# Performance work log

Hardware: AMD Instinct MI355X
Metric: run time of the kernel (lower is better)

The kernel has to match this reference:

```python
import jax, jax.numpy as jnp
import numpy as np

NEG_INF = -1e30  # stand-in for -inf that is safe under softmax
HEADS = 16


def slice_diag_idx(t):
    # result[i, j] = matrix[i, i + j] for matrix of shape (..., t, 2t-1)
    rows = jnp.arange(t)
    cols = rows[:, None] + rows[None, :]  # (t, t), values in [0, 2t-2]
    return rows, cols


def setup_inputs() -> dict:
    key = jax.random.key(0)
    ks = jax.random.split(key, 10)
    b, t, e, h = 4, 1024, 1024, HEADS
    s = e // h
    sc = 0.02
    return {
        "x": jax.random.normal(ks[0], (b, t, e), jnp.float32),
        "Wq": jax.random.normal(ks[1], (e, e), jnp.float32) * sc,
        "Wk": jax.random.normal(ks[2], (e, e), jnp.float32) * sc,
        "Wkp": jax.random.normal(ks[3], (e, e), jnp.float32) * sc,
        "Wv": jax.random.normal(ks[4], (e, e), jnp.float32) * sc,
        "Wu": jax.random.normal(ks[5], (e, e), jnp.float32) * sc,
        "bu": jax.random.normal(ks[6], (e,), jnp.float32) * sc,
        "parma": jax.random.normal(ks[7], (1, h, 1, s), jnp.float32),
        "parmb": jax.random.normal(ks[8], (1, h, 1, s), jnp.float32),
        "pos_emb": jax.random.normal(ks[9], (2 * t - 1, e), jnp.float32),
    }


def reference(x, Wq, Wk, Wkp, Wv, Wu, bu, parma, parmb, pos_emb):
    b, t, e = x.shape
    h = HEADS
    s = e // h

    q = (x @ Wq).reshape(b, t, h, s).transpose(0, 2, 1, 3)   # (b,h,t,s)
    k = (x @ Wk).reshape(b, t, h, s).transpose(0, 2, 1, 3)   # (b,h,t,s)
    v = (x @ Wv).reshape(b, t, h, s).transpose(0, 2, 1, 3)   # (b,h,t,s)
    # positions are identical across batch -> compute once, shape (2t-1,h,s)
    kp = (pos_emb @ Wkp).reshape(2 * t - 1, h, s)

    pa = parma[0, :, 0, :]  # (h,s), broadcast over query position i
    pb = parmb[0, :, 0, :]  # (h,s)

    rows, cols = slice_diag_idx(t)

    # content-content
    dot_tt = jnp.einsum('bhis,bhjs->bhij', q, k)                 # (b,h,t,t)
    # content-position, then slice_diag: [i,j] -> [i, i+j]
    dot_tp_full = jnp.einsum('bhis,jhs->bhij', q, kp)            # (b,h,t,2t-1)
    dot_tp = dot_tp_full[:, :, rows[:, None], cols]              # (b,h,t,t)
    # position-content: constant over query index i
    dot_pt = jnp.einsum('hs,bhjs->bhj', pa, k)[:, :, None, :]    # (b,h,1,t)
    # position-position: constant over i before slicing; slice gives c[i+j]
    c_pp = jnp.einsum('hs,jhs->hj', pb, kp)                      # (h,2t-1)
    dot_pp = c_pp[:, cols][None]                                 # (1,h,t,t)

    dot = dot_tt + dot_tp + dot_pt + dot_pp                      # (b,h,t,t)

    # causal mask: strict upper triangle (j > i) -> -inf
    causal = rows[:, None] >= rows[None, :]                      # (t,t)
    dot = jnp.where(causal[None, None], dot, NEG_INF)

    att = jax.nn.softmax(dot, axis=-1)
    out = jnp.einsum('bhij,bhjs->bhis', att, v)                  # (b,h,t,s)
    out = out.transpose(0, 2, 1, 3).reshape(b, t, e)
    return out @ Wu + bu
```

## Files before the change

kernel.cpp:

```cpp
#include <hip/hip_runtime.h>

typedef unsigned short u16;
typedef unsigned int   u32;
using bf16x8 = __attribute__((ext_vector_type(8))) __bf16;
using f32x4  = __attribute__((ext_vector_type(4))) float;
using u16x8  = __attribute__((ext_vector_type(8))) u16;

#define NEG_INF_F (-1e30f)

__device__ __forceinline__ u16 f2bf(float f) {
  u32 u = __float_as_uint(f);
  u32 r = (u + 0x7FFFu + ((u >> 16) & 1u)) >> 16;
  return (u16)r;
}

__device__ __forceinline__ void async_copy16(const void* g, void* lds) {
  __builtin_amdgcn_global_load_lds(
      (const __attribute__((address_space(1))) void*)g,
      (__attribute__((address_space(3))) void*)lds, 16, 0, 0);
}

__global__ __launch_bounds__(256) void cvt_bf16(const float* __restrict__ in,
                                                u16* __restrict__ out, int n4) {
  int i = blockIdx.x * 256 + threadIdx.x;
  if (i >= n4) return;
  float4 v = reinterpret_cast<const float4*>(in)[i];
  u16 o0 = f2bf(v.x), o1 = f2bf(v.y), o2 = f2bf(v.z), o3 = f2bf(v.w);
  ushort4 o = {o0, o1, o2, o3};
  reinterpret_cast<ushort4*>(out)[i] = o;
}

__global__ __launch_bounds__(256) void cvt_w_tr(
    const float* __restrict__ w0, const float* __restrict__ w1,
    const float* __restrict__ w2, const float* __restrict__ w3,
    const float* __restrict__ w4,
    u16* __restrict__ o0, u16* __restrict__ o1, u16* __restrict__ o2,
    u16* __restrict__ o3, u16* __restrict__ o4) {
  __shared__ float tile[64][65];
  const float* src; u16* dst;
  switch (blockIdx.z) {
    case 0: src = w0; dst = o0; break;
    case 1: src = w1; dst = o1; break;
    case 2: src = w2; dst = o2; break;
    case 3: src = w3; dst = o3; break;
    default: src = w4; dst = o4; break;
  }
  const int tid = threadIdx.x;
  const int r0 = blockIdx.y * 64;
  const int c0 = blockIdx.x * 64;
#pragma unroll
  for (int i = 0; i < 16; ++i) {
    int lin = tid + i * 256;
    int r = lin >> 6, c = lin & 63;
    tile[r][c] = src[(size_t)(r0 + r) * 1024 + c0 + c];
  }
  __syncthreads();
#pragma unroll
  for (int i = 0; i < 16; ++i) {
    int lin = tid + i * 256;
    int n = lin >> 6, k = lin & 63;
    dst[(size_t)(c0 + n) * 1024 + r0 + k] = f2bf(tile[k][n]);
  }
}

__global__ __launch_bounds__(512, 2) void gemm_qkvp(
    const u16* __restrict__ x_bf, const u16* __restrict__ pos_bf,
    const u16* __restrict__ BtQKV, const u16* __restrict__ BtKP,
    u16* __restrict__ qa, u16* __restrict__ qb, u16* __restrict__ kb,
    u16* __restrict__ vb, u16* __restrict__ kp,
    const float* __restrict__ parma, const float* __restrict__ parmb) {
  const int bx = blockIdx.x, by = blockIdx.y;
  const bool isKP = bx >= 24;
  if (isKP && by >= 16) return;

  __shared__ u16 As[128 * 64];
  __shared__ u16 Bs[128 * 64];
  const int tid = threadIdx.x;
  const int w = tid >> 6, l = tid & 63;
  const int lg = l >> 4, lc = l & 15;
  const int wr = w >> 2, wc = w & 3;
  const u16* A  = isKP ? pos_bf : x_bf;
  const u16* Bt = isKP ? BtKP : BtQKV;
  const int M = isKP ? 2047 : 4096;
  const int row0 = by * 128;
  const int col0 = (isKP ? (bx - 24) : bx) * 128;

  f32x4 acc[4][2];
#pragma unroll
  for (int fi = 0; fi < 4; ++fi)
#pragma unroll
    for (int fj = 0; fj < 2; ++fj) acc[fi][fj] = (f32x4){0.f, 0.f, 0.f, 0.f};

  for (int kbk = 0; kbk < 1024; kbk += 64) {
#pragma unroll
    for (int it2 = 0; it2 < 2; ++it2) {
      int seg = w * 2 + it2;
      int r = seg * 8 + (l >> 3);
      int c8 = (l & 7) * 8;
      int gr = row0 + r; if (gr > M - 1) gr = M - 1;
      async_copy16(&A[(size_t)gr * 1024 + kbk + c8], &As[seg * 512]);
      async_copy16(&Bt[(size_t)(col0 + r) * 1024 + kbk + c8], &Bs[seg * 512]);
    }
    __syncthreads();
#pragma unroll
    for (int ks = 0; ks < 2; ++ks) {
      bf16x8 af[4], bfr[2];
#pragma unroll
      for (int fi = 0; fi < 4; ++fi)
        af[fi] = *reinterpret_cast<const bf16x8*>(
            &As[(wr * 64 + fi * 16 + lc) * 64 + ks * 32 + lg * 8]);
#pragma unroll
      for (int fj = 0; fj < 2; ++fj)
        bfr[fj] = *reinterpret_cast<const bf16x8*>(
            &Bs[(wc * 32 + fj * 16 + lc) * 64 + ks * 32 + lg * 8]);
#pragma unroll
      for (int fi = 0; fi < 4; ++fi)
#pragma unroll
        for (int fj = 0; fj < 2; ++fj)
          acc[fi][fj] = __builtin_amdgcn_mfma_f32_16x16x32_bf16(
              af[fi], bfr[fj], acc[fi][fj], 0, 0, 0);
    }
    __syncthreads();
  }

#pragma unroll
  for (int fi = 0; fi < 4; ++fi)
#pragma unroll
    for (int fj = 0; fj < 2; ++fj)
#pragma unroll
      for (int reg = 0; reg < 4; ++reg) {
        int R = row0 + wr * 64 + fi * 16 + lg * 4 + reg;
        int C = col0 + wc * 32 + fj * 16 + lc;
        float val = acc[fi][fj][reg];
        if (isKP) {
          if (R < 2047) {
            int hh = C >> 6, ss = C & 63;
            kp[((size_t)hh * 2047 + R) * 64 + ss] = f2bf(val);
          }
        } else {
          int wsel = C >> 10, Cl = C & 1023;
          int bi = R >> 10, tt = R & 1023, hh = Cl >> 6, ss = Cl & 63;
          size_t o = ((size_t)(bi * 16 + hh) << 16) + (size_t)tt * 64 + ss;
          if (wsel == 0) {
            qa[o] = f2bf(val + parma[Cl]);
            qb[o] = f2bf(val + parmb[Cl]);
          } else if (wsel == 1) {
            kb[o] = f2bf(val);
          } else {
            vb[o] = f2bf(val);
          }
        }
      }
}

__global__ __launch_bounds__(512, 2) void gemm_out(
    const u16* __restrict__ A, const u16* __restrict__ Bt,
    float* __restrict__ outF, const float* __restrict__ bias) {
  __shared__ u16 As[128 * 64];
  __shared__ u16 Bs[128 * 64];
  const int tid = threadIdx.x;
  const int w = tid >> 6, l = tid & 63;
  const int lg = l >> 4, lc = l & 15;
  const int wr = w >> 2, wc = w & 3;
  const int row0 = blockIdx.y * 128;
  const int col0 = blockIdx.x * 128;

  f32x4 acc[4][2];
#pragma unroll
  for (int fi = 0; fi < 4; ++fi)
#pragma unroll
    for (int fj = 0; fj < 2; ++fj) acc[fi][fj] = (f32x4){0.f, 0.f, 0.f, 0.f};

  for (int kbk = 0; kbk < 1024; kbk += 64) {
#pragma unroll
    for (int it2 = 0; it2 < 2; ++it2) {
      int seg = w * 2 + it2;
      int r = seg * 8 + (l >> 3);
      int c8 = (l & 7) * 8;
      async_copy16(&A[(size_t)(row0 + r) * 1024 + kbk + c8], &As[seg * 512]);
      async_copy16(&Bt[(size_t)(col0 + r) * 1024 + kbk + c8], &Bs[seg * 512]);
    }
    __syncthreads();
#pragma unroll
    for (int ks = 0; ks < 2; ++ks) {
      bf16x8 af[4], bfr[2];
#pragma unroll
      for (int fi = 0; fi < 4; ++fi)
        af[fi] = *reinterpret_cast<const bf16x8*>(
            &As[(wr * 64 + fi * 16 + lc) * 64 + ks * 32 + lg * 8]);
#pragma unroll
      for (int fj = 0; fj < 2; ++fj)
        bfr[fj] = *reinterpret_cast<const bf16x8*>(
            &Bs[(wc * 32 + fj * 16 + lc) * 64 + ks * 32 + lg * 8]);
#pragma unroll
      for (int fi = 0; fi < 4; ++fi)
#pragma unroll
        for (int fj = 0; fj < 2; ++fj)
          acc[fi][fj] = __builtin_amdgcn_mfma_f32_16x16x32_bf16(
              af[fi], bfr[fj], acc[fi][fj], 0, 0, 0);
    }
    __syncthreads();
  }

#pragma unroll
  for (int fi = 0; fi < 4; ++fi)
#pragma unroll
    for (int fj = 0; fj < 2; ++fj)
#pragma unroll
      for (int reg = 0; reg < 4; ++reg) {
        int R = row0 + wr * 64 + fi * 16 + lg * 4 + reg;
        int C = col0 + wc * 32 + fj * 16 + lc;
        outF[(size_t)R * 1024 + C] = acc[fi][fj][reg] + bias[C];
      }
}

__global__ __launch_bounds__(512, 2) void attn_mfma(
    const u16* __restrict__ qa_g, const u16* __restrict__ qb_g,
    const u16* __restrict__ k_g, const u16* __restrict__ v_g,
    const u16* __restrict__ kp_g, u16* __restrict__ ctx) {
  __shared__ u16 kT[64 * 72];
  __shared__ u16 vT[64 * 72];
  __shared__ u16 kpl[192 * 72];
  __shared__ float G[8][16 * 81];
  __shared__ u16 P[8][16 * 72];

  const int tid = threadIdx.x;
  const int w = tid >> 6, l = tid & 63;
  const int lg = l >> 4, lc = l & 15;
  const int bh = blockIdx.x;
  const int h = bh & 15;
  const int i0 = (7 - (int)blockIdx.y) * 128;
  const size_t bhOff = (size_t)bh << 16;
  const size_t hOff = (size_t)h * 2047 * 64;

  bf16x8 qaf[2], qbf[2];
#pragma unroll
  for (int ks = 0; ks < 2; ++ks) {
    size_t o = bhOff + (size_t)(i0 + w * 16 + lc) * 64 + ks * 32 + lg * 8;
    qaf[ks] = *reinterpret_cast<const bf16x8*>(&qa_g[o]);
    qbf[ks] = *reinterpret_cast<const bf16x8*>(&qb_g[o]);
  }

  const int k_j = tid >> 3, k_c8 = (tid & 7) * 8;
  const int v_j = tid & 63, v_s0 = (tid >> 6) * 8;
  u16x8 pk, pv, pp[3];
  {
    pk = *reinterpret_cast<const u16x8*>(&k_g[bhOff + (size_t)k_j * 64 + k_c8]);
    pv = *reinterpret_cast<const u16x8*>(&v_g[bhOff + (size_t)v_j * 64 + v_s0]);
#pragma unroll
    for (int r = 0; r < 3; ++r) {
      int idx = tid + r * 512;
      int d = idx >> 3, c8 = (idx & 7) * 8;
      int p = i0 + d; if (p > 2046) p = 2046;
      pp[r] = *reinterpret_cast<const u16x8*>(&kp_g[hOff + (size_t)p * 64 + c8]);
    }
  }

  f32x4 O[4];
  float m_r[4], l_r[4];
#pragma unroll
  for (int fj = 0; fj < 4; ++fj) O[fj] = (f32x4){0.f, 0.f, 0.f, 0.f};
#pragma unroll
  for (int reg = 0; reg < 4; ++reg) { m_r[reg] = NEG_INF_F; l_r[reg] = 0.f; }

  const int nt = (i0 >> 6) + 2;
  for (int jt = 0; jt < nt; ++jt) {
    const int j0 = jt * 64;
    __syncthreads();
    *reinterpret_cast<u16x8*>(&kT[k_j * 72 + k_c8]) = pk;
#pragma unroll
    for (int i2 = 0; i2 < 8; ++i2) vT[(v_s0 + i2) * 72 + v_j] = pv[i2];
#pragma unroll
    for (int r = 0; r < 3; ++r) {
      int idx = tid + r * 512;
      int d = idx >> 3, c8 = (idx & 7) * 8;
      *reinterpret_cast<u16x8*>(&kpl[d * 72 + c8]) = pp[r];
    }
    __syncthreads();
    if (jt + 1 < nt) {
      const int jn = j0 + 64, pbn = i0 + jn;
      pk = *reinterpret_cast<const u16x8*>(
          &k_g[bhOff + (size_t)(jn + k_j) * 64 + k_c8]);
      pv = *reinterpret_cast<const u16x8*>(
          &v_g[bhOff + (size_t)(jn + v_j) * 64 + v_s0]);
#pragma unroll
      for (int r = 0; r < 3; ++r) {
        int idx = tid + r * 512;
        int d = idx >> 3, c8 = (idx & 7) * 8;
        int p = pbn + d; if (p > 2046) p = 2046;
        pp[r] = *reinterpret_cast<const u16x8*>(&kp_g[hOff + (size_t)p * 64 + c8]);
      }
    }
    if (j0 > i0 + w * 16 + 15) continue;

    f32x4 S[4], Gf[5];
#pragma unroll
    for (int fj = 0; fj < 4; ++fj) S[fj] = (f32x4){0.f, 0.f, 0.f, 0.f};
#pragma unroll
    for (int fg = 0; fg < 5; ++fg) Gf[fg] = (f32x4){0.f, 0.f, 0.f, 0.f};
#pragma unroll
    for (int ks = 0; ks < 2; ++ks) {
#pragma unroll
      for (int fj = 0; fj < 4; ++fj) {
        bf16x8 kf = *reinterpret_cast<const bf16x8*>(
            &kT[(fj * 16 + lc) * 72 + ks * 32 + lg * 8]);
        S[fj] = __builtin_amdgcn_mfma_f32_16x16x32_bf16(qaf[ks], kf, S[fj], 0, 0, 0);
      }
#pragma unroll
      for (int fg = 0; fg < 5; ++fg) {
        bf16x8 pf = *reinterpret_cast<const bf16x8*>(
            &kpl[((w + fg) * 16 + lc) * 72 + ks * 32 + lg * 8]);
        Gf[fg] = __builtin_amdgcn_mfma_f32_16x16x32_bf16(qbf[ks], pf, Gf[fg], 0, 0, 0);
      }
    }
    float* Gw = G[w];
#pragma unroll
    for (int fg = 0; fg < 5; ++fg)
#pragma unroll
      for (int reg = 0; reg < 4; ++reg)
        Gw[(lg * 4 + reg) * 81 + fg * 16 + lc] = Gf[fg][reg];
    asm volatile("s_waitcnt lgkmcnt(0)" ::: "memory");
    __builtin_amdgcn_sched_barrier(0);
    const bool needMask = (j0 + 63 > i0 + w * 16);
#pragma unroll
    for (int fj = 0; fj < 4; ++fj)
#pragma unroll
      for (int reg = 0; reg < 4; ++reg) {
        int rf = lg * 4 + reg;
        float sv = S[fj][reg] + Gw[rf * 81 + rf + fj * 16 + lc];
        if (needMask && (i0 + w * 16 + rf) < (j0 + fj * 16 + lc)) sv = NEG_INF_F;
        S[fj][reg] = sv;
      }
#pragma unroll
    for (int reg = 0; reg < 4; ++reg) {
      float mx = fmaxf(fmaxf(S[0][reg], S[1][reg]), fmaxf(S[2][reg], S[3][reg]));
      mx = fmaxf(mx, __shfl_xor(mx, 1));
      mx = fmaxf(mx, __shfl_xor(mx, 2));
      mx = fmaxf(mx, __shfl_xor(mx, 4));
      mx = fmaxf(mx, __shfl_xor(mx, 8));
      float mnew = fmaxf(m_r[reg], mx);
      float corr = __expf(m_r[reg] - mnew);
      float rs = 0.f;
#pragma unroll
      for (int fj = 0; fj < 4; ++fj) {
        float p = __expf(S[fj][reg] - mnew);
        S[fj][reg] = p;
        rs += p;
      }
      rs += __shfl_xor(rs, 1); rs += __shfl_xor(rs, 2);
      rs += __shfl_xor(rs, 4); rs += __shfl_xor(rs, 8);
      l_r[reg] = l_r[reg] * corr + rs;
      m_r[reg] = mnew;
#pragma unroll
      for (int fj = 0; fj < 4; ++fj) O[fj][reg] *= corr;
    }
    u16* Pw = P[w];
#pragma unroll
    for (int fj = 0; fj < 4; ++fj)
#pragma unroll
      for (int reg = 0; reg < 4; ++reg)
        Pw[(lg * 4 + reg) * 72 + fj * 16 + lc] = f2bf(S[fj][reg]);
    asm volatile("s_waitcnt lgkmcnt(0)" ::: "memory");
    __builtin_amdgcn_sched_barrier(0);
#pragma unroll
    for (int ks = 0; ks < 2; ++ks) {
      bf16x8 pa = *reinterpret_cast<const bf16x8*>(&Pw[lc * 72 + ks * 32 + lg * 8]);
#pragma unroll
      for (int fj = 0; fj < 4; ++fj) {
        bf16x8 vb = *reinterpret_cast<const bf16x8*>(
            &vT[(fj * 16 + lc) * 72 + ks * 32 + lg * 8]);
        O[fj] = __builtin_amdgcn_mfma_f32_16x16x32_bf16(pa, vb, O[fj], 0, 0, 0);
      }
    }
  }

  const int b = bh >> 4;
#pragma unroll
  for (int reg = 0; reg < 4; ++reg) {
    float inv = 1.f / l_r[reg];
    int r = w * 16 + lg * 4 + reg;
#pragma unroll
    for (int fj = 0; fj < 4; ++fj)
      ctx[((size_t)b * 1024 + i0 + r) * 1024 + h * 64 + fj * 16 + lc] =
          f2bf(O[fj][reg] * inv);
  }
}

extern "C" void kernel_launch(void* const* d_in, const int* in_sizes, int n_in,
                              void* d_out, int out_size, void* d_ws, size_t ws_size,
                              hipStream_t stream) {
  const float* x       = (const float*)d_in[0];
  const float* Wq      = (const float*)d_in[1];
  const float* Wk      = (const float*)d_in[2];
  const float* Wkp     = (const float*)d_in[3];
  const float* Wv      = (const float*)d_in[4];
  const float* Wu      = (const float*)d_in[5];
  const float* bu      = (const float*)d_in[6];
  const float* parma   = (const float*)d_in[7];
  const float* parmb   = (const float*)d_in[8];
  const float* pos_emb = (const float*)d_in[9];
  float* out = (float*)d_out;

  u16* W = (u16*)d_ws;
  u16* x_bf   = W;
  u16* pos_bf = x_bf + 4194304;
  u16* wqT    = pos_bf + 2096128;
  u16* wkT    = wqT + 1048576;
  u16* wvT    = wkT + 1048576;
  u16* wkpT   = wvT + 1048576;
  u16* wuT    = wkpT + 1048576;
  u16* qa     = wuT + 1048576;
  u16* qb     = qa + 4194304;
  u16* kb     = qb + 4194304;
  u16* vb     = kb + 4194304;
  u16* kp     = vb + 4194304;
  u16* ctx    = kp + 2096128;

  cvt_bf16<<<4096, 256, 0, stream>>>(x, x_bf, 1048576);
  cvt_bf16<<<2047, 256, 0, stream>>>(pos_emb, pos_bf, 524032);
  cvt_w_tr<<<dim3(16, 16, 5), 256, 0, stream>>>(Wq, Wk, Wkp, Wv, Wu,
                                                wqT, wkT, wkpT, wvT, wuT);
  gemm_qkvp<<<dim3(32, 32), 512, 0, stream>>>(x_bf, pos_bf, wqT, wkpT,
                                              qa, qb, kb, vb, kp, parma, parmb);
  attn_mfma<<<dim3(64, 8), 512, 0, stream>>>(qa, qb, kb, vb, kp, ctx);
  gemm_out<<<dim3(8, 32), 512, 0, stream>>>(ctx, wuT, out, bu);
}
```

Before: 252.8 us.

## Enlarge QKV/KP GEMM tiles to 256x256 with double-buffered swizzled LDS

Rewrites the projection GEMM to use 256x256 output tiles per block, giving each wave 8x4 MFMA fragments. It adds double-buffered async global-to-LDS staging with explicit vmcnt waits, and an XOR swizzle on the LDS layout to avoid bank conflicts. The 2D grid, which had idle KP blocks, becomes a flat 224-block grid. The aim is more data reuse per LDS load and overlap of loads with MFMA work, at the cost of 128KB LDS per block (one block per CU), fewer blocks than CUs, and heavier register use.

```diff
diff --git a/kernel.cpp b/kernel.cpp
--- a/kernel.cpp
+++ b/kernel.cpp
@@ -63,74 +63,106 @@
   }
 }
 
+__device__ __forceinline__ void stage_tile(const u16* __restrict__ gsrc,
+                                           int row0, int kbk, int maxRow,
+                                           u16* lds, int tid) {
+  const int lane = tid & 63;
+  const int wchunk = (tid >> 6) * 64;
+#pragma unroll
+  for (int r4 = 0; r4 < 4; ++r4) {
+    int cbase = wchunk + r4 * 512;
+    int c = cbase + lane;
+    int row = c >> 3, cc = c & 7;
+    int scc = cc ^ (row & 7);
+    int gr = row0 + row; if (gr > maxRow) gr = maxRow;
+    async_copy16(&gsrc[(size_t)gr * 1024 + kbk + scc * 8],
+                 lds + (size_t)cbase * 8);
+  }
+}
+
 __global__ __launch_bounds__(512, 2) void gemm_qkvp(
     const u16* __restrict__ x_bf, const u16* __restrict__ pos_bf,
     const u16* __restrict__ BtQKV, const u16* __restrict__ BtKP,
     u16* __restrict__ qa, u16* __restrict__ qb, u16* __restrict__ kb,
     u16* __restrict__ vb, u16* __restrict__ kp,
     const float* __restrict__ parma, const float* __restrict__ parmb) {
-  const int bx = blockIdx.x, by = blockIdx.y;
-  const bool isKP = bx >= 24;
-  if (isKP && by >= 16) return;
-
-  __shared__ u16 As[128 * 64];
-  __shared__ u16 Bs[128 * 64];
+  __shared__ __align__(16) u16 As[2][256 * 64];
+  __shared__ __align__(16) u16 Bs[2][256 * 64];
+
   const int tid = threadIdx.x;
   const int w = tid >> 6, l = tid & 63;
   const int lg = l >> 4, lc = l & 15;
   const int wr = w >> 2, wc = w & 3;
-  const u16* A  = isKP ? pos_bf : x_bf;
-  const u16* Bt = isKP ? BtKP : BtQKV;
-  const int M = isKP ? 2047 : 4096;
-  const int row0 = by * 128;
-  const int col0 = (isKP ? (bx - 24) : bx) * 128;
-
-  f32x4 acc[4][2];
-#pragma unroll
-  for (int fi = 0; fi < 4; ++fi)
-#pragma unroll
-    for (int fj = 0; fj < 2; ++fj) acc[fi][fj] = (f32x4){0.f, 0.f, 0.f, 0.f};
-
-  for (int kbk = 0; kbk < 1024; kbk += 64) {
-#pragma unroll
-    for (int it2 = 0; it2 < 2; ++it2) {
-      int seg = w * 2 + it2;
-      int r = seg * 8 + (l >> 3);
-      int c8 = (l & 7) * 8;
-      int gr = row0 + r; if (gr > M - 1) gr = M - 1;
-      async_copy16(&A[(size_t)gr * 1024 + kbk + c8], &As[seg * 512]);
-      async_copy16(&Bt[(size_t)(col0 + r) * 1024 + kbk + c8], &Bs[seg * 512]);
-    }
-    __syncthreads();
+  const int bid = blockIdx.x;
+  const bool isKP = bid >= 192;
+  int row0, col0;
+  const u16 *A, *Bt;
+  int maxRowA, maxRowB;
+  if (!isKP) {
+    int by = bid / 12, bx = bid - by * 12;
+    row0 = by * 256; col0 = bx * 256;
+    A = x_bf; Bt = BtQKV; maxRowA = 4095; maxRowB = 3071;
+  } else {
+    int idx = bid - 192;
+    int by = idx >> 2, bx = idx & 3;
+    row0 = by * 256; col0 = bx * 256;
+    A = pos_bf; Bt = BtKP; maxRowA = 2046; maxRowB = 1023;
+  }
+
+  f32x4 acc[8][4];
+#pragma unroll
+  for (int fi = 0; fi < 8; ++fi)
+#pragma unroll
+    for (int fj = 0; fj < 4; ++fj) acc[fi][fj] = (f32x4){0.f, 0.f, 0.f, 0.f};
+
+  stage_tile(A, row0, 0, maxRowA, &As[0][0], tid);
+  stage_tile(Bt, col0, 0, maxRowB, &Bs[0][0], tid);
+
+  const int NT = 16;
+  for (int t = 0; t < NT; ++t) {
+    const int cur = t & 1;
+    if (t + 1 < NT) {
+      stage_tile(A, row0, (t + 1) * 64, maxRowA, &As[cur ^ 1][0], tid);
+      stage_tile(Bt, col0, (t + 1) * 64, maxRowB, &Bs[cur ^ 1][0], tid);
+      asm volatile("s_waitcnt vmcnt(8)" ::: "memory");
+    } else {
+      asm volatile("s_waitcnt vmcnt(0)" ::: "memory");
+    }
+    __builtin_amdgcn_s_barrier();
+    __builtin_amdgcn_sched_barrier(0);
+
+    const u16* bufA = &As[cur][0];
+    const u16* bufB = &Bs[cur][0];
 #pragma unroll
     for (int ks = 0; ks < 2; ++ks) {
-      bf16x8 af[4], bfr[2];
-#pragma unroll
-      for (int fi = 0; fi < 4; ++fi)
-        af[fi] = *reinterpret_cast<const bf16x8*>(
-            &As[(wr * 64 + fi * 16 + lc) * 64 + ks * 32 + lg * 8]);
-#pragma unroll
-      for (int fj = 0; fj < 2; ++fj)
-        bfr[fj] = *reinterpret_cast<const bf16x8*>(
-            &Bs[(wc * 32 + fj * 16 + lc) * 64 + ks * 32 + lg * 8]);
-#pragma unroll
-      for (int fi = 0; fi < 4; ++fi)
-#pragma unroll
-        for (int fj = 0; fj < 2; ++fj)
+      const int pc = ((ks << 2) | lg) ^ (lc & 7);
+      const u16* pA = bufA + (wr * 128 + lc) * 64 + pc * 8;
+      const u16* pB = bufB + (wc * 64 + lc) * 64 + pc * 8;
+      bf16x8 af[8], bfr[4];
+#pragma unroll
+      for (int fi = 0; fi < 8; ++fi)
+        af[fi] = *reinterpret_cast<const bf16x8*>(pA + fi * 1024);
+#pragma unroll
+      for (int fj = 0; fj < 4; ++fj)
+        bfr[fj] = *reinterpret_cast<const bf16x8*>(pB + fj * 1024);
+#pragma unroll
+      for (int fi = 0; fi < 8; ++fi)
+#pragma unroll
+        for (int fj = 0; fj < 4; ++fj)
           acc[fi][fj] = __builtin_amdgcn_mfma_f32_16x16x32_bf16(
               af[fi], bfr[fj], acc[fi][fj], 0, 0, 0);
     }
-    __syncthreads();
-  }
-
-#pragma unroll
-  for (int fi = 0; fi < 4; ++fi)
-#pragma unroll
-    for (int fj = 0; fj < 2; ++fj)
+    __builtin_amdgcn_s_barrier();
+  }
+
+#pragma unroll
+  for (int fi = 0; fi < 8; ++fi)
+#pragma unroll
+    for (int fj = 0; fj < 4; ++fj)
 #pragma unroll
       for (int reg = 0; reg < 4; ++reg) {
-        int R = row0 + wr * 64 + fi * 16 + lg * 4 + reg;
-        int C = col0 + wc * 32 + fj * 16 + lc;
+        int R = row0 + wr * 128 + fi * 16 + lg * 4 + reg;
+        int C = col0 + wc * 64 + fj * 16 + lc;
         float val = acc[fi][fj][reg];
         if (isKP) {
           if (R < 2047) {
@@ -420,8 +452,8 @@
   cvt_bf16<<<2047, 256, 0, stream>>>(pos_emb, pos_bf, 524032);
   cvt_w_tr<<<dim3(16, 16, 5), 256, 0, stream>>>(Wq, Wk, Wkp, Wv, Wu,
                                                 wqT, wkT, wkpT, wvT, wuT);
-  gemm_qkvp<<<dim3(32, 32), 512, 0, stream>>>(x_bf, pos_bf, wqT, wkpT,
-                                              qa, qb, kb, vb, kp, parma, parmb);
+  gemm_qkvp<<<224, 512, 0, stream>>>(x_bf, pos_bf, wqT, wkpT,
+                                     qa, qb, kb, vb, kp, parma, parmb);
   attn_mfma<<<dim3(64, 8), 512, 0, stream>>>(qa, qb, kb, vb, kp, ctx);
   gemm_out<<<dim3(8, 32), 512, 0, stream>>>(ctx, wuT, out, bu);
 }
```

Measured after the change: 250.2 us. No clear change (-1.0%).
